# Kernel optimization log

Measured on AMD Instinct MI355X. Metric: run time of the kernel, lower is better.

## Reference

```python
import jax, jax.numpy as jnp
import numpy as np

DIM = 1024
NUM_HEADS = 16
HEAD_DIM = DIM // NUM_HEADS
SCALE = HEAD_DIM ** -0.5


def setup_inputs() -> dict:
    key = jax.random.key(0)
    k1, k2, k3 = jax.random.split(key, 3)
    B, N = 2, 2048
    x = jax.random.normal(k1, (B, N, DIM), dtype=jnp.float32)
    W_qkv = jax.random.normal(k2, (DIM, 3 * DIM), dtype=jnp.float32) * (DIM ** -0.5)
    b_qkv = jnp.zeros((3 * DIM,), dtype=jnp.float32)
    W_proj = jax.random.normal(k3, (DIM, DIM), dtype=jnp.float32) * (DIM ** -0.5)
    b_proj = jnp.zeros((DIM,), dtype=jnp.float32)
    return {"x": x, "W_qkv": W_qkv, "b_qkv": b_qkv, "W_proj": W_proj, "b_proj": b_proj}


def reference(x, W_qkv, b_qkv, W_proj, b_proj):
    B, N, D = x.shape
    qkv = x @ W_qkv + b_qkv                      # [B, N, 3D]
    qkv = qkv.reshape(B, N, 3, NUM_HEADS, HEAD_DIM)
    qkv = jnp.transpose(qkv, (2, 0, 3, 1, 4))    # [3, B, H, N, hd]
    q, k, v = qkv[0], qkv[1], qkv[2]
    attn = jnp.einsum('bhqd,bhkd->bhqk', q, k) * SCALE  # [B, H, N, N]
    attn = jax.nn.softmax(attn, axis=-1)
    out = jnp.einsum('bhqk,bhkd->bhqd', attn, v)        # [B, H, N, hd]
    out = jnp.transpose(out, (0, 2, 1, 3)).reshape(B, N, D)
    out = out @ W_proj + b_proj
    return out
```

## Files before the change

kernel.cpp:

```cpp
#include <hip/hip_runtime.h>


typedef __bf16 bf16_t;
typedef __bf16 bf16x2 __attribute__((ext_vector_type(2)));
typedef __bf16 bf16x4 __attribute__((ext_vector_type(4)));
typedef __bf16 bf16x8 __attribute__((ext_vector_type(8)));
typedef float  f32x4  __attribute__((ext_vector_type(4)));

#define NTOK 2048
#define DIM  1024
#define NH   16
#define HD   64
#define SCL2 0.18033688011112042f

#define MFMA16(a, b, c) __builtin_amdgcn_mfma_f32_16x16x32_bf16((a), (b), (c), 0, 0, 0)

__device__ __forceinline__ void gload_lds16(const void* g, void* l) {
  __builtin_amdgcn_global_load_lds((const __attribute__((address_space(1))) void*)g,
                                   (__attribute__((address_space(3))) void*)l, 16, 0, 0);
}

__device__ __forceinline__ void transpose_cvt_tile(const float* __restrict__ W,
                                                   bf16_t* __restrict__ WT,
                                                   int cols, int bx, int by) {
  __shared__ float tile[32][33];
  int j0 = bx * 32, i0 = by * 32;
  int c = threadIdx.x & 31, r0 = threadIdx.x >> 5;
#pragma unroll
  for (int it = 0; it < 4; ++it) {
    int r = r0 + it * 8;
    tile[r][c] = W[(long)(i0 + r) * cols + j0 + c];
  }
  __syncthreads();
#pragma unroll
  for (int it = 0; it < 4; ++it) {
    int r = r0 + it * 8;
    int orow = j0 + r, ocol = i0 + c;
    WT[(long)orow * 1024 + ((((ocol >> 3) ^ (orow & 7)) << 3) | (ocol & 7))] =
        (bf16_t)tile[c][r];
  }
}

__global__ __launch_bounds__(256) void k_prep(const float* __restrict__ x,
                                              bf16_t* __restrict__ xb,
                                              const float* __restrict__ Wq,
                                              bf16_t* __restrict__ WqT,
                                              const float* __restrict__ Wp,
                                              bf16_t* __restrict__ WpT) {
  int id = blockIdx.x;
  if (id < 2048) {
    int i = (id * 256 + threadIdx.x) * 8;
    float4 a = *(const float4*)(x + i);
    float4 b = *(const float4*)(x + i + 4);
    bf16x8 v;
    v[0] = (bf16_t)a.x; v[1] = (bf16_t)a.y; v[2] = (bf16_t)a.z; v[3] = (bf16_t)a.w;
    v[4] = (bf16_t)b.x; v[5] = (bf16_t)b.y; v[6] = (bf16_t)b.z; v[7] = (bf16_t)b.w;
    int r = i >> 10, c = (i & 1023) >> 3;
    *(bf16x8*)(xb + r * 1024 + ((c ^ (r & 7)) << 3)) = v;
  } else if (id < 2048 + 3072) {
    int t = id - 2048;
    transpose_cvt_tile(Wq, WqT, 3072, t % 96, t / 96);
  } else {
    int t = id - 5120;
    transpose_cvt_tile(Wp, WpT, 1024, t & 31, t >> 5);
  }
}

__device__ __forceinline__ void gemm_core(const bf16_t* __restrict__ A,
                                          const bf16_t* __restrict__ B,
                                          int K, int bm, int bn,
                                          bf16_t* As, bf16_t* Bs, f32x4 acc[4][4]) {
  const int t = threadIdx.x;
  const int lane = t & 63;
  const int w = t >> 6;
  const int wr = (w >> 1) * 64, wc = (w & 1) * 64;
  const int l15 = lane & 15, g = lane >> 4;
  const int srow = t >> 3, scol = (t & 7) * 8;
  const f32x4 vzero = {0.f, 0.f, 0.f, 0.f};
#pragma unroll
  for (int m = 0; m < 4; ++m)
#pragma unroll
    for (int n = 0; n < 4; ++n) acc[m][n] = vzero;

  const bf16_t* ga = A + (long)(bm + srow) * K + scol;
  const bf16_t* gb = B + (long)(bn + srow) * K + scol;
  bf16_t* lA = As + srow * 64 + scol;
  bf16_t* lB = Bs + srow * 64 + scol;
  const int xr = l15 & 7;

  auto stageAB = [&](int buf, int k0) {
#pragma unroll
    for (int j = 0; j < 4; ++j) {
      gload_lds16(ga + (long)32 * j * K + k0, lA + buf * 8192 + j * 2048);
      gload_lds16(gb + (long)32 * j * K + k0, lB + buf * 8192 + j * 2048);
    }
  };

  const int nsteps = K >> 6;
  stageAB(0, 0);
  stageAB(1, 64);

  for (int s = 0; s < nsteps; ++s) {
    if (s == nsteps - 1) asm volatile("s_waitcnt vmcnt(0)" ::: "memory");
    else                 asm volatile("s_waitcnt vmcnt(8)" ::: "memory");
    __builtin_amdgcn_s_barrier();
    const char* Ab = (const char*)(As + (s & 1) * 8192);
    const char* Bb = (const char*)(Bs + (s & 1) * 8192);
#pragma unroll
    for (int kk = 0; kk < 2; ++kk) {
      bf16x8 af[4], bfv[4];
#pragma unroll
      for (int m = 0; m < 4; ++m)
        af[m] = *(const bf16x8*)(Ab + (wr + m * 16 + l15) * 128 +
                                 (((kk * 4 + g) ^ xr) << 4));
#pragma unroll
      for (int n = 0; n < 4; ++n)
        bfv[n] = *(const bf16x8*)(Bb + (wc + n * 16 + l15) * 128 +
                                  (((kk * 4 + g) ^ xr) << 4));
#pragma unroll
      for (int m = 0; m < 4; ++m)
#pragma unroll
        for (int n = 0; n < 4; ++n)
          acc[m][n] = MFMA16(af[m], bfv[n], acc[m][n]);
    }
    __builtin_amdgcn_s_barrier();
    if (s + 2 < nsteps) stageAB(s & 1, (s + 2) * 64);
  }
}

__global__ __launch_bounds__(256) void k_gemm_qkv(const bf16_t* __restrict__ xb,
                                                  const bf16_t* __restrict__ WqT,
                                                  const float* __restrict__ bq,
                                                  bf16_t* __restrict__ Qb,
                                                  bf16_t* __restrict__ Kb,
                                                  bf16_t* __restrict__ Vt) {
  __shared__ alignas(16) bf16_t As[2 * 128 * 64];
  __shared__ alignas(16) bf16_t Bs[2 * 128 * 64];
  f32x4 acc[4][4];
  const int bid = blockIdx.x;
  const int xcd = bid & 7, ib = bid >> 3;
  const int bn = (xcd * 3 + (ib >> 5)) * 128;
  const int bm = (ib & 31) * 128;
  gemm_core(xb, WqT, DIM, bm, bn, As, Bs, acc);

  const int lane = threadIdx.x & 63, w = threadIdx.x >> 6;
  const int wr = (w >> 1) * 64, wc = (w & 1) * 64;
  const int l15 = lane & 15, g = lane >> 4;
#pragma unroll
  for (int n = 0; n < 4; ++n) {
    int col = bn + wc + n * 16 + l15;
    float bias = bq[col];
    int t3 = col >> 10, rem = col & 1023;
    int h = rem >> 6, d = rem & 63;
#pragma unroll
    for (int m = 0; m < 4; ++m) {
      int rowb = bm + wr + m * 16 + g * 4;
#pragma unroll
      for (int r = 0; r < 4; ++r) {
        int row = rowb + r;
        int b = row >> 11, tok = row & 2047;
        int bh = b * NH + h;
        float val = acc[m][n][r] + bias;
        if (t3 == 0) {
          Qb[bh * (NTOK * HD) + tok * HD + d] = (bf16_t)(val * SCL2);
        } else if (t3 == 1) {
          int rr = tok & 63;
          int off = bh * (NTOK * HD) + (tok >> 6) * 4096 + rr * 64 +
                    (((d >> 3) ^ (rr & 7)) << 3) + (d & 7);
          Kb[off] = (bf16_t)val;
        } else {
          int ct = tok & 63;
          int off = bh * (NTOK * HD) + (tok >> 6) * 4096 + d * 64 +
                    (((ct >> 3) ^ (d & 7)) << 3) + (ct & 7);
          Vt[off] = (bf16_t)val;
        }
      }
    }
  }
}

__global__ __launch_bounds__(256, 3) void k_attn(const bf16_t* __restrict__ Qb,
                                                 const bf16_t* __restrict__ Kb,
                                                 const bf16_t* __restrict__ Vt,
                                                 bf16_t* __restrict__ Ob) {
  __shared__ alignas(16) bf16_t Ks[2][64 * 64];
  __shared__ alignas(16) bf16_t Vs[2][64 * 64];
  __shared__ alignas(16) char  P2[4][4096];

  const int b0 = blockIdx.x;
  const int swz = (b0 & 7) * 64 + (b0 >> 3);
  const int qt = swz & 15, bh = swz >> 4;
  const int b = bh >> 4, h = bh & 15;
  const int t = threadIdx.x;
  const int w = t >> 6, lane = t & 63;
  const int l15 = lane & 15, g = lane >> 4;
  const bf16_t* Qp = Qb + bh * (NTOK * HD);
  const bf16_t* Kp = Kb + bh * (NTOK * HD);
  const bf16_t* Vp = Vt + bh * (NTOK * HD);
  const int q0 = qt * 128 + w * 32;
  char* P2w = &P2[w][0];

  const int cs0 = ((g ^ (l15 & 7)) << 4);
  const int cs1 = cs0 ^ 64;

  bf16x8 qfr[2][2];
#pragma unroll
  for (int qf = 0; qf < 2; ++qf)
#pragma unroll
    for (int kk = 0; kk < 2; ++kk)
      qfr[qf][kk] = *(const bf16x8*)(Qp + (q0 + qf * 16 + l15) * HD + kk * 32 + g * 8);

  bf16x8 ones;
#pragma unroll
  for (int i = 0; i < 8; ++i) ones[i] = (bf16_t)1.0f;

  const f32x4 vzero = {0.f, 0.f, 0.f, 0.f};
  f32x4 o[2][4];
#pragma unroll
  for (int qf = 0; qf < 2; ++qf)
#pragma unroll
    for (int df = 0; df < 4; ++df) o[qf][df] = vzero;
  f32x4 o_sum[2] = {vzero, vzero};

  auto stage = [&](int buf, int tile) {
    const bf16_t* gk = Kp + tile * 4096 + t * 8;
    const bf16_t* gv = Vp + tile * 4096 + t * 8;
    gload_lds16(gk,        (char*)Ks[buf] + t * 16);
    gload_lds16(gk + 2048, (char*)Ks[buf] + 4096 + t * 16);
    gload_lds16(gv,        (char*)Vs[buf] + t * 16);
    gload_lds16(gv + 2048, (char*)Vs[buf] + 4096 + t * 16);
  };

  stage(0, 0);
  stage(1, 1);

  for (int i = 0; i < 32; ++i) {
    if (i == 31) asm volatile("s_waitcnt vmcnt(0)" ::: "memory");
    else         asm volatile("s_waitcnt vmcnt(4)" ::: "memory");
    __builtin_amdgcn_s_barrier();
    const char* kbuf = (const char*)Ks[i & 1];
    const char* vbuf = (const char*)Vs[i & 1];
    f32x4 s[2][4];
    __builtin_amdgcn_s_setprio(1);
#pragma unroll
    for (int kf = 0; kf < 4; ++kf) {
      int rb = (kf * 16 + l15) * 128;
      bf16x8 ka0 = *(const bf16x8*)(kbuf + rb + cs0);
      bf16x8 ka1 = *(const bf16x8*)(kbuf + rb + cs1);
      s[0][kf] = MFMA16(ka0, qfr[0][0], vzero);
      s[1][kf] = MFMA16(ka0, qfr[1][0], vzero);
      s[0][kf] = MFMA16(ka1, qfr[0][1], s[0][kf]);
      s[1][kf] = MFMA16(ka1, qfr[1][1], s[1][kf]);
    }
    __builtin_amdgcn_s_setprio(0);
#pragma unroll
    for (int qf = 0; qf < 2; ++qf)
#pragma unroll
      for (int kf = 0; kf < 4; ++kf) {
        bf16x4 pw;
        pw[0] = (bf16_t)__builtin_amdgcn_exp2f(s[qf][kf][0]);
        pw[1] = (bf16_t)__builtin_amdgcn_exp2f(s[qf][kf][1]);
        pw[2] = (bf16_t)__builtin_amdgcn_exp2f(s[qf][kf][2]);
        pw[3] = (bf16_t)__builtin_amdgcn_exp2f(s[qf][kf][3]);
        *(bf16x4*)(P2w + qf * 2048 + (2 * kf + (g >> 1)) * 256 + l15 * 16 + 8 * (g & 1)) = pw;
      }
    __builtin_amdgcn_s_setprio(1);
#pragma unroll
    for (int kb = 0; kb < 2; ++kb) {
      bf16x8 pf0 = *(const bf16x8*)(P2w + kb * 1024 + lane * 16);
      bf16x8 pf1 = *(const bf16x8*)(P2w + 2048 + kb * 1024 + lane * 16);
      int csk = kb ? cs1 : cs0;
      o_sum[0] = MFMA16(ones, pf0, o_sum[0]);
      o_sum[1] = MFMA16(ones, pf1, o_sum[1]);
#pragma unroll
      for (int df = 0; df < 4; ++df) {
        bf16x8 va = *(const bf16x8*)(vbuf + (df * 16 + l15) * 128 + csk);
        o[0][df] = MFMA16(va, pf0, o[0][df]);
        o[1][df] = MFMA16(va, pf1, o[1][df]);
      }
    }
    __builtin_amdgcn_s_setprio(0);
    __builtin_amdgcn_s_barrier();
    if (i + 2 < 32) stage(i & 1, i + 2);
  }
#pragma unroll
  for (int qf = 0; qf < 2; ++qf) {
    float inv = 1.0f / o_sum[qf][0];
    int tok = q0 + qf * 16 + l15;
    bf16_t* oprow = Ob + (long)(b * NTOK + tok) * DIM;
    const int xr = l15 & 7;
#pragma unroll
    for (int df = 0; df < 4; ++df) {
#pragma unroll
      for (int rp = 0; rp < 2; ++rp) {
        bf16x2 v2;
        v2[0] = (bf16_t)(o[qf][df][rp * 2]     * inv);
        v2[1] = (bf16_t)(o[qf][df][rp * 2 + 1] * inv);
        int c = h * 8 + df * 2 + (g >> 1);
        *(bf16x2*)(oprow + ((c ^ xr) << 3) + (g & 1) * 4 + rp * 2) = v2;
      }
    }
  }
}

__global__ __launch_bounds__(256) void k_gemm_proj(const bf16_t* __restrict__ Ob,
                                                   const bf16_t* __restrict__ WpT,
                                                   const float* __restrict__ bp,
                                                   float* __restrict__ out) {
  __shared__ alignas(16) bf16_t As[2 * 128 * 64];
  __shared__ alignas(16) bf16_t Bs[2 * 128 * 64];
  f32x4 acc[4][4];
  const int bid = blockIdx.x;
  const int bn = (bid & 7) * 128;
  const int bm = (bid >> 3) * 128;
  gemm_core(Ob, WpT, DIM, bm, bn, As, Bs, acc);

  const int lane = threadIdx.x & 63, w = threadIdx.x >> 6;
  const int wr = (w >> 1) * 64, wc = (w & 1) * 64;
  const int l15 = lane & 15, g = lane >> 4;
#pragma unroll
  for (int n = 0; n < 4; ++n) {
    int col = bn + wc + n * 16 + l15;
    float bias = bp[col];
#pragma unroll
    for (int m = 0; m < 4; ++m) {
      int rowb = bm + wr + m * 16 + g * 4;
#pragma unroll
      for (int r = 0; r < 4; ++r)
        out[(long)(rowb + r) * DIM + col] = acc[m][n][r] + bias;
    }
  }
}

extern "C" void kernel_launch(void* const* d_in, const int* in_sizes, int n_in,
                              void* d_out, int out_size, void* d_ws, size_t ws_size,
                              hipStream_t stream) {
  const float* x     = (const float*)d_in[0];
  const float* Wqkv  = (const float*)d_in[1];
  const float* bqkv  = (const float*)d_in[2];
  const float* Wproj = (const float*)d_in[3];
  const float* bproj = (const float*)d_in[4];
  float* out = (float*)d_out;

  char* ws = (char*)d_ws;
  bf16_t* xb  = (bf16_t*)(ws);
  bf16_t* WqT = (bf16_t*)(ws + (8l  << 20));
  bf16_t* WpT = (bf16_t*)(ws + (14l << 20));
  bf16_t* Qb  = (bf16_t*)(ws + (16l << 20));
  bf16_t* Kb  = (bf16_t*)(ws + (24l << 20));
  bf16_t* Vt  = (bf16_t*)(ws + (32l << 20));
  bf16_t* Ob  = (bf16_t*)(ws);

  k_prep<<<6144, 256, 0, stream>>>(x, xb, Wqkv, WqT, Wproj, WpT);
  k_gemm_qkv<<<768, 256, 0, stream>>>(xb, WqT, bqkv, Qb, Kb, Vt);
  k_attn<<<512, 256, 0, stream>>>(Qb, Kb, Vt, Ob);
  k_gemm_proj<<<256, 256, 0, stream>>>(Ob, WpT, bproj, out);
}
```

Baseline: 121.1 us.

## Rewrite QKV GEMM as 256x256 tile, 8-wave, finely interleaved pipeline

The QKV projection GEMM moves from 128x128 tiles with 4 waves to 256x256 tiles with 8 waves (192 blocks of 512 threads). Global-to-LDS staging is split into quarter-tile events interleaved between sub-MFMA phases, with barriers, MFMA priority raising and tuned vmcnt waits. The goal is more data reuse per block and better overlap of loads with matrix math. In exchange it uses 128 KB of LDS and more registers, and only 192 blocks may underfill the 256 CUs.

```diff
diff --git a/kernel.cpp b/kernel.cpp
--- a/kernel.cpp
+++ b/kernel.cpp
@@ -14,6 +14,8 @@
 #define SCL2 0.18033688011112042f
 
 #define MFMA16(a, b, c) __builtin_amdgcn_mfma_f32_16x16x32_bf16((a), (b), (c), 0, 0, 0)
+#define BAR()   __builtin_amdgcn_s_barrier()
+#define LGKM0() asm volatile("s_waitcnt lgkmcnt(0)" ::: "memory")
 
 __device__ __forceinline__ void gload_lds16(const void* g, void* l) {
   __builtin_amdgcn_global_load_lds((const __attribute__((address_space(1))) void*)g,
@@ -66,100 +68,130 @@
   }
 }
 
-__device__ __forceinline__ void gemm_core(const bf16_t* __restrict__ A,
-                                          const bf16_t* __restrict__ B,
-                                          int K, int bm, int bn,
-                                          bf16_t* As, bf16_t* Bs, f32x4 acc[4][4]) {
+__global__ __launch_bounds__(512, 2) void k_gemm_qkv(const bf16_t* __restrict__ xb,
+                                                     const bf16_t* __restrict__ WqT,
+                                                     const float* __restrict__ bq,
+                                                     bf16_t* __restrict__ Qb,
+                                                     bf16_t* __restrict__ Kb,
+                                                     bf16_t* __restrict__ Vt) {
+  __shared__ alignas(16) bf16_t As[2][256 * 64];
+  __shared__ alignas(16) bf16_t Bs[2][256 * 64];
   const int t = threadIdx.x;
-  const int lane = t & 63;
-  const int w = t >> 6;
-  const int wr = (w >> 1) * 64, wc = (w & 1) * 64;
+  const int w = t >> 6, lane = t & 63;
   const int l15 = lane & 15, g = lane >> 4;
-  const int srow = t >> 3, scol = (t & 7) * 8;
-  const f32x4 vzero = {0.f, 0.f, 0.f, 0.f};
-#pragma unroll
-  for (int m = 0; m < 4; ++m)
-#pragma unroll
-    for (int n = 0; n < 4; ++n) acc[m][n] = vzero;
-
-  const bf16_t* ga = A + (long)(bm + srow) * K + scol;
-  const bf16_t* gb = B + (long)(bn + srow) * K + scol;
-  bf16_t* lA = As + srow * 64 + scol;
-  bf16_t* lB = Bs + srow * 64 + scol;
+  const int wm = w >> 2, wn = w & 3;
   const int xr = l15 & 7;
 
-  auto stageAB = [&](int buf, int k0) {
-#pragma unroll
-    for (int j = 0; j < 4; ++j) {
-      gload_lds16(ga + (long)32 * j * K + k0, lA + buf * 8192 + j * 2048);
-      gload_lds16(gb + (long)32 * j * K + k0, lB + buf * 8192 + j * 2048);
-    }
-  };
-
-  const int nsteps = K >> 6;
-  stageAB(0, 0);
-  stageAB(1, 64);
-
-  for (int s = 0; s < nsteps; ++s) {
-    if (s == nsteps - 1) asm volatile("s_waitcnt vmcnt(0)" ::: "memory");
-    else                 asm volatile("s_waitcnt vmcnt(8)" ::: "memory");
-    __builtin_amdgcn_s_barrier();
-    const char* Ab = (const char*)(As + (s & 1) * 8192);
-    const char* Bb = (const char*)(Bs + (s & 1) * 8192);
-#pragma unroll
-    for (int kk = 0; kk < 2; ++kk) {
-      bf16x8 af[4], bfv[4];
-#pragma unroll
-      for (int m = 0; m < 4; ++m)
-        af[m] = *(const bf16x8*)(Ab + (wr + m * 16 + l15) * 128 +
-                                 (((kk * 4 + g) ^ xr) << 4));
-#pragma unroll
-      for (int n = 0; n < 4; ++n)
-        bfv[n] = *(const bf16x8*)(Bb + (wc + n * 16 + l15) * 128 +
-                                  (((kk * 4 + g) ^ xr) << 4));
-#pragma unroll
-      for (int m = 0; m < 4; ++m)
-#pragma unroll
-        for (int n = 0; n < 4; ++n)
-          acc[m][n] = MFMA16(af[m], bfv[n], acc[m][n]);
-    }
-    __builtin_amdgcn_s_barrier();
-    if (s + 2 < nsteps) stageAB(s & 1, (s + 2) * 64);
-  }
-}
-
-__global__ __launch_bounds__(256) void k_gemm_qkv(const bf16_t* __restrict__ xb,
-                                                  const bf16_t* __restrict__ WqT,
-                                                  const float* __restrict__ bq,
-                                                  bf16_t* __restrict__ Qb,
-                                                  bf16_t* __restrict__ Kb,
-                                                  bf16_t* __restrict__ Vt) {
-  __shared__ alignas(16) bf16_t As[2 * 128 * 64];
-  __shared__ alignas(16) bf16_t Bs[2 * 128 * 64];
-  f32x4 acc[4][4];
   const int bid = blockIdx.x;
   const int xcd = bid & 7, ib = bid >> 3;
-  const int bn = (xcd * 3 + (ib >> 5)) * 128;
-  const int bm = (ib & 31) * 128;
-  gemm_core(xb, WqT, DIM, bm, bn, As, Bs, acc);
-
-  const int lane = threadIdx.x & 63, w = threadIdx.x >> 6;
-  const int wr = (w >> 1) * 64, wc = (w & 1) * 64;
-  const int l15 = lane & 15, g = lane >> 4;
+  const int bm = ((xcd & 3) * 4 + (ib & 3)) * 256;
+  const int bn = ((xcd >> 2) * 6 + (ib >> 2)) * 256;
+
+  const bf16_t* Ag = xb + (long)bm * 1024;
+  const bf16_t* Bg = WqT + (long)bn * 1024;
+
+  auto st1 = [&](bf16_t* lds, const bf16_t* gsrc, int row0, int kt) {
+    gload_lds16(gsrc + (long)(row0 + (t >> 3)) * 1024 + kt * 64 + (t & 7) * 8,
+                (char*)lds + row0 * 128 + t * 16);
+  };
+  auto evA = [&](int slot, int kt, int half) {
+    st1(As[slot], Ag, half * 64, kt);
+    st1(As[slot], Ag, half * 64 + 128, kt);
+  };
+  auto evB = [&](int slot, int kt, int half) {
+    st1(Bs[slot], Bg, half * 128, kt);
+    st1(Bs[slot], Bg, half * 128 + 64, kt);
+  };
+
+  f32x4 acc[8][4];
+  const f32x4 vzero = {0.f, 0.f, 0.f, 0.f};
+#pragma unroll
+  for (int m = 0; m < 8; ++m)
+#pragma unroll
+    for (int n = 0; n < 4; ++n) acc[m][n] = vzero;
+
+  bf16x8 bf[4][2], af[4][2];
+  auto ldB = [&](int slot) {
+#pragma unroll
+    for (int n = 0; n < 4; ++n)
+#pragma unroll
+      for (int kk = 0; kk < 2; ++kk)
+        bf[n][kk] = *(const bf16x8*)((const char*)Bs[slot] +
+                    (wn * 64 + n * 16 + l15) * 128 + (((kk * 4 + g) ^ xr) << 4));
+  };
+  auto ldA = [&](int slot, int half) {
+#pragma unroll
+    for (int m = 0; m < 4; ++m)
+#pragma unroll
+      for (int kk = 0; kk < 2; ++kk)
+        af[m][kk] = *(const bf16x8*)((const char*)As[slot] +
+                    (wm * 128 + half * 64 + m * 16 + l15) * 128 +
+                    (((kk * 4 + g) ^ xr) << 4));
+  };
+  auto mma = [&](int mb, int nb) {
+    __builtin_amdgcn_s_setprio(1);
+#pragma unroll
+    for (int m = 0; m < 4; ++m)
+#pragma unroll
+      for (int n = 0; n < 2; ++n)
+#pragma unroll
+        for (int kk = 0; kk < 2; ++kk)
+          acc[mb + m][nb + n] = MFMA16(af[m][kk], bf[nb + n][kk], acc[mb + m][nb + n]);
+    __builtin_amdgcn_s_setprio(0);
+  };
+
+  evB(0, 0, 0); evB(0, 0, 1); evA(0, 0, 0); evA(0, 0, 1);
+  evB(1, 1, 0); evB(1, 1, 1); evA(1, 1, 0);
+  asm volatile("s_waitcnt vmcnt(6)" ::: "memory");
+  BAR();
+
+  for (int it = 0; it < 8; ++it) {
+    const bool stg = it < 7;
+#pragma unroll
+    for (int h = 0; h < 2; ++h) {
+      const int tile = 2 * it + h;
+      ldB(h); ldA(h, 0);
+      if (h == 0)      evA(1, tile + 1, 1);
+      else if (stg)    evA(0, tile + 1, 1);
+      BAR(); LGKM0();
+      mma(0, 0);
+      BAR();
+      if (stg) evB(h, tile + 2, 0);
+      BAR(); LGKM0();
+      mma(0, 2);
+      BAR();
+      ldA(h, 1);
+      if (stg) evB(h, tile + 2, 1);
+      BAR(); LGKM0();
+      mma(4, 0);
+      BAR();
+      if (stg) evA(h, tile + 2, 0);
+      if (h == 0) {
+        if (stg) asm volatile("s_waitcnt vmcnt(6)" ::: "memory");
+        else     asm volatile("s_waitcnt vmcnt(0)" ::: "memory");
+      } else if (stg) {
+        asm volatile("s_waitcnt vmcnt(6)" ::: "memory");
+      }
+      BAR(); LGKM0();
+      mma(4, 2);
+      BAR();
+    }
+  }
+
 #pragma unroll
   for (int n = 0; n < 4; ++n) {
-    int col = bn + wc + n * 16 + l15;
+    int col = bn + wn * 64 + n * 16 + l15;
     float bias = bq[col];
     int t3 = col >> 10, rem = col & 1023;
-    int h = rem >> 6, d = rem & 63;
-#pragma unroll
-    for (int m = 0; m < 4; ++m) {
-      int rowb = bm + wr + m * 16 + g * 4;
+    int hh = rem >> 6, d = rem & 63;
+#pragma unroll
+    for (int m = 0; m < 8; ++m) {
+      int rowb = bm + wm * 128 + m * 16 + g * 4;
 #pragma unroll
       for (int r = 0; r < 4; ++r) {
         int row = rowb + r;
         int b = row >> 11, tok = row & 2047;
-        int bh = b * NH + h;
+        int bh = b * NH + hh;
         float val = acc[m][n][r] + bias;
         if (t3 == 0) {
           Qb[bh * (NTOK * HD) + tok * HD + d] = (bf16_t)(val * SCL2);
@@ -179,6 +211,68 @@
   }
 }
 
+__device__ __forceinline__ void gemm_core(const bf16_t* __restrict__ A,
+                                          const bf16_t* __restrict__ B,
+                                          int K, int bm, int bn,
+                                          bf16_t* As, bf16_t* Bs, f32x4 acc[4][4]) {
+  const int t = threadIdx.x;
+  const int lane = t & 63;
+  const int w = t >> 6;
+  const int wr = (w >> 1) * 64, wc = (w & 1) * 64;
+  const int l15 = lane & 15, g = lane >> 4;
+  const int srow = t >> 3, scol = (t & 7) * 8;
+  const f32x4 vzero = {0.f, 0.f, 0.f, 0.f};
+#pragma unroll
+  for (int m = 0; m < 4; ++m)
+#pragma unroll
+    for (int n = 0; n < 4; ++n) acc[m][n] = vzero;
+
+  const bf16_t* ga = A + (long)(bm + srow) * K + scol;
+  const bf16_t* gb = B + (long)(bn + srow) * K + scol;
+  bf16_t* lA = As + srow * 64 + scol;
+  bf16_t* lB = Bs + srow * 64 + scol;
+  const int xr = l15 & 7;
+
+  auto stageAB = [&](int buf, int k0) {
+#pragma unroll
+    for (int j = 0; j < 4; ++j) {
+      gload_lds16(ga + (long)32 * j * K + k0, lA + buf * 8192 + j * 2048);
+      gload_lds16(gb + (long)32 * j * K + k0, lB + buf * 8192 + j * 2048);
+    }
+  };
+
+  const int nsteps = K >> 6;
+  stageAB(0, 0);
+  stageAB(1, 64);
+
+  for (int s = 0; s < nsteps; ++s) {
+    if (s == nsteps - 1) asm volatile("s_waitcnt vmcnt(0)" ::: "memory");
+    else                 asm volatile("s_waitcnt vmcnt(8)" ::: "memory");
+    __builtin_amdgcn_s_barrier();
+    const char* Ab = (const char*)(As + (s & 1) * 8192);
+    const char* Bb = (const char*)(Bs + (s & 1) * 8192);
+#pragma unroll
+    for (int kk = 0; kk < 2; ++kk) {
+      bf16x8 af[4], bfv[4];
+#pragma unroll
+      for (int m = 0; m < 4; ++m)
+        af[m] = *(const bf16x8*)(Ab + (wr + m * 16 + l15) * 128 +
+                                 (((kk * 4 + g) ^ xr) << 4));
+#pragma unroll
+      for (int n = 0; n < 4; ++n)
+        bfv[n] = *(const bf16x8*)(Bb + (wc + n * 16 + l15) * 128 +
+                                  (((kk * 4 + g) ^ xr) << 4));
+#pragma unroll
+      for (int m = 0; m < 4; ++m)
+#pragma unroll
+        for (int n = 0; n < 4; ++n)
+          acc[m][n] = MFMA16(af[m], bfv[n], acc[m][n]);
+    }
+    __builtin_amdgcn_s_barrier();
+    if (s + 2 < nsteps) stageAB(s & 1, (s + 2) * 64);
+  }
+}
+
 __global__ __launch_bounds__(256, 3) void k_attn(const bf16_t* __restrict__ Qb,
                                                  const bf16_t* __restrict__ Kb,
                                                  const bf16_t* __restrict__ Vt,
@@ -352,7 +446,7 @@
   bf16_t* Ob  = (bf16_t*)(ws);
 
   k_prep<<<6144, 256, 0, stream>>>(x, xb, Wqkv, WqT, Wproj, WpT);
-  k_gemm_qkv<<<768, 256, 0, stream>>>(xb, WqT, bqkv, Qb, Kb, Vt);
+  k_gemm_qkv<<<192, 512, 0, stream>>>(xb, WqT, bqkv, Qb, Kb, Vt);
   k_attn<<<512, 256, 0, stream>>>(Qb, Kb, Vt, Ob);
   k_gemm_proj<<<256, 256, 0, stream>>>(Ob, WpT, bproj, out);
 }
```

Result: faster. 117.9 us (-2.6%).
